# Kernel optimization log

Measured on AMD Instinct MI355X. Metric: run time of the kernel, lower is better.

The kernel has to match this reference:

```python
import jax, jax.numpy as jnp
import numpy as np
from jax import lax

TOP_K = 2

def _unfold(x_img, k):
    # F.unfold(kernel=k, stride=k): [B,C,H,W] -> [B, C*k*k, L], column index c*k*k + kh*k + kw
    B, C, H, W = x_img.shape
    Hp, Wp = H // k, W // k
    u = x_img.reshape(B, C, Hp, k, Wp, k).transpose(0, 1, 3, 5, 2, 4)
    return u.reshape(B, C * k * k, Hp * Wp)

def _fold(p, k, H, W):
    # F.fold inverse of non-overlapping unfold: [B, C*k*k, L] -> [B,C,H,W]
    B = p.shape[0]
    C = p.shape[1] // (k * k)
    Hp, Wp = H // k, W // k
    u = p.reshape(B, C, k, k, Hp, Wp).transpose(0, 1, 4, 2, 5, 3)
    return u.reshape(B, C, H, W)

def setup_inputs() -> dict:
    key = jax.random.key(0)
    ks = jax.random.split(key, 6)
    B, H, W, C, F, E, P = 8, 64, 64, 384, 1536, 8, 4
    N = H * W
    x = jax.random.normal(ks[0], (B, N, C), dtype=jnp.float32)
    gate_w = jax.random.normal(ks[1], (E, C, P, P), dtype=jnp.float32) * 0.01
    w1 = jax.random.normal(ks[2], (E, C, F), dtype=jnp.float32) * (1.0 / np.sqrt(C))
    b1 = jax.random.normal(ks[3], (E, F), dtype=jnp.float32) * 0.01
    w2 = jax.random.normal(ks[4], (E, F, C), dtype=jnp.float32) * (1.0 / np.sqrt(F))
    b2 = jax.random.normal(ks[5], (E, C), dtype=jnp.float32) * 0.01
    return {"x": x, "gate_w": gate_w, "w1": w1, "b1": b1, "w2": w2, "b2": b2, "H": H, "W": W}

def reference(x, gate_w, w1, b1, w2, b2, H, W):
    B, N, C = x.shape
    E, _, P, _ = gate_w.shape
    k2 = P * P
    Hp, Wp = H // P, W // P
    L = Hp * Wp
    x_img = jnp.transpose(x, (0, 2, 1)).reshape(B, C, H, W)
    # router: strided conv -> logits per patch
    logits_map = lax.conv_general_dilated(
        x_img, gate_w, window_strides=(P, P), padding='VALID',
        dimension_numbers=('NCHW', 'OIHW', 'NCHW'))  # [B,E,Hp,Wp]
    router_logits = jnp.transpose(logits_map, (0, 2, 3, 1)).reshape(B, L, E)
    probs = jax.nn.softmax(router_logits, axis=-1)
    ew, ei = lax.top_k(probs, TOP_K)  # [B,L,topk]
    ew = ew / (jnp.sum(ew, axis=-1, keepdims=True) + 1e-9)
    # expand to token level (faithful to original's reshape/flatten ordering)
    ei_tok = jnp.broadcast_to(ei[:, :, None, :], (B, L, k2, TOP_K)).reshape(-1, TOP_K)
    ew_tok = jnp.broadcast_to(ew[:, :, None, :], (B, L, k2, TOP_K)).reshape(-1, TOP_K)
    # unfold + the original's (scrambled) reshape(B, C, L, k2)
    U = _unfold(x_img, P)  # [B, C*k2, L]
    x_patches = jnp.transpose(U.reshape(B, C, L, k2), (0, 2, 3, 1))  # [B,L,k2,C]
    flat_x = x_patches.reshape(-1, C)  # [T,C], T = B*L*k2
    # combine weights: zero for experts not in top-k == masked dispatch math
    cw = jnp.zeros((flat_x.shape[0], E), dtype=flat_x.dtype)
    for kk in range(TOP_K):
        cw = cw + jax.nn.one_hot(ei_tok[:, kk], E, dtype=flat_x.dtype) * ew_tok[:, kk:kk + 1]
    out = jnp.zeros_like(flat_x)
    for e in range(E):
        h = jax.nn.gelu(flat_x @ w1[e] + b1[e], approximate=False)
        y = h @ w2[e] + b2[e]
        out = out + cw[:, e:e + 1] * y
    # fold back (mirrors original's reshape/permute exactly)
    o = jnp.transpose(out.reshape(B, L, k2, C), (0, 3, 1, 2)).reshape(B, C * k2, L)
    out_img = _fold(o, P, H, W)  # [B,C,H,W]
    # original: output.transpose(1,2).reshape(B,N,C) on NCHW tensor
    output = jnp.transpose(out_img, (0, 2, 1, 3)).reshape(B, N, C)
    return output
```

## Files before the change

### kernel.cpp

```cpp
#include <hip/hip_runtime.h>
#include <hip/hip_bf16.h>

#define BB   8
#define HH   64
#define WWID 64
#define CC   384
#define FF   1536
#define EE   8
#define LL   256
#define MTOTMAX 66560
#define NTMAX   520

typedef unsigned short ushort_t;
typedef __attribute__((ext_vector_type(4))) unsigned short u16x4;
typedef __attribute__((ext_vector_type(8))) short          s16x8;
typedef __attribute__((ext_vector_type(4))) float          f32x4;

__device__ __forceinline__ float bf2f(ushort_t u) {
  union { unsigned int i; float f; } v; v.i = ((unsigned int)u) << 16; return v.f;
}
__device__ __forceinline__ ushort_t f2bf(float f) {
  union { float f; unsigned int i; } v; v.f = f;
  unsigned int u = v.i;
  u += 0x7fffu + ((u >> 16) & 1u);
  return (ushort_t)(u >> 16);
}
__device__ __forceinline__ float gelu_f(float x) {
  float u  = 0.70710678118654752f * x;
  float au = fabsf(u);
  float t  = 1.0f / (1.0f + 0.3275911f * au);
  float poly = t * (0.254829592f + t * (-0.284496736f + t * (1.421413741f +
               t * (-1.453152027f + t * 1.061405429f))));
  float ea = 1.0f - poly * __expf(-au * au);
  float erfv = (x < 0.f) ? -ea : ea;
  return 0.5f * x * (1.0f + erfv);
}

#define GLDS(g, l) __builtin_amdgcn_global_load_lds( \
    (const __attribute__((address_space(1))) void*)(g), \
    (__attribute__((address_space(3))) void*)(l), 16, 0, 0)

__global__ __launch_bounds__(256) void k_transpose(const float* __restrict__ src,
                                                   ushort_t* __restrict__ dst,
                                                   int R, int Cd) {
  __shared__ ushort_t tile[32][33];
  int e  = blockIdx.z;
  int c0 = blockIdx.x * 32, r0 = blockIdx.y * 32;
  int tx = threadIdx.x & 31, ty = threadIdx.x >> 5;
  const float* s = src + (size_t)e * R * Cd;
  ushort_t*    d = dst + (size_t)e * R * Cd;
  #pragma unroll
  for (int i = 0; i < 32; i += 8)
    tile[ty + i][tx] = f2bf(s[(size_t)(r0 + ty + i) * Cd + c0 + tx]);
  __syncthreads();
  #pragma unroll
  for (int i = 0; i < 32; i += 8)
    d[(size_t)(c0 + ty + i) * R + r0 + tx] = tile[tx][ty + i];
}

__global__ __launch_bounds__(256) void k_router(const float* __restrict__ x,
                                                const float* __restrict__ gw,
                                                int* __restrict__ re, float* __restrict__ rw,
                                                int* __restrict__ cnt) {
  int bid = blockIdx.x;
  int b = bid >> 8, l2 = bid & 255;
  int hp = l2 >> 4, wp = l2 & 15;
  int t = threadIdx.x;
  int e = t >> 5, lane = t & 31;
  const float* xb = x + (size_t)b * (HH * WWID) * CC;
  const float* ge = gw + (size_t)e * CC * 16;
  float acc = 0.f;
  for (int c = lane; c < CC; c += 32) {
    const float* gp = ge + c * 16;
    #pragma unroll
    for (int kh = 0; kh < 4; ++kh) {
      const float* xr = xb + (size_t)((hp * 4 + kh) * 64 + wp * 4) * CC + c;
      #pragma unroll
      for (int kw = 0; kw < 4; ++kw)
        acc += xr[(size_t)kw * CC] * gp[kh * 4 + kw];
    }
  }
  #pragma unroll
  for (int d = 16; d; d >>= 1) acc += __shfl_down(acc, d, 32);
  __shared__ float logits[EE];
  if (lane == 0) logits[e] = acc;
  __syncthreads();
  if (t == 0) {
    float m = logits[0];
    #pragma unroll
    for (int i = 1; i < EE; ++i) m = fmaxf(m, logits[i]);
    float p[EE]; float s = 0.f;
    #pragma unroll
    for (int i = 0; i < EE; ++i) { p[i] = __expf(logits[i] - m); s += p[i]; }
    #pragma unroll
    for (int i = 0; i < EE; ++i) p[i] /= s;
    int e0 = 0;
    #pragma unroll
    for (int i = 1; i < EE; ++i) if (p[i] > p[e0]) e0 = i;
    int e1 = (e0 == 0) ? 1 : 0;
    #pragma unroll
    for (int i = 0; i < EE; ++i) if (i != e0 && p[i] > p[e1]) e1 = i;
    float s2 = p[e0] + p[e1] + 1e-9f;
    re[bid * 2 + 0] = e0;  re[bid * 2 + 1] = e1;
    rw[bid * 2 + 0] = p[e0] / s2;  rw[bid * 2 + 1] = p[e1] / s2;
    atomicAdd(&cnt[e0], 16);
    atomicAdd(&cnt[e1], 16);
  }
}

__global__ void k_pad(const int* __restrict__ cnt, int* __restrict__ cntp,
                      int* __restrict__ basep, int* __restrict__ tile2e,
                      int* __restrict__ gids, float* __restrict__ gwts) {
  __shared__ int s_cnt[EE], s_cntp[EE], s_base[EE + 1];
  int t = threadIdx.x;
  if (t == 0) {
    int b = 0;
    for (int e = 0; e < EE; ++e) {
      int c  = cnt[e];
      int cp = (c + 127) & ~127;
      s_cnt[e] = c; s_cntp[e] = cp; s_base[e] = b;
      b += cp;
    }
    s_base[EE] = b;
  }
  __syncthreads();
  if (t < EE) { cntp[t] = s_cntp[t]; basep[t] = s_base[t]; }
  if (t == EE) basep[EE] = s_base[EE];
  int ntot = s_base[EE] >> 7;
  for (int g = t; g < ntot; g += 256) {
    int e = 0;
    #pragma unroll
    for (int i = 1; i < EE; ++i) if (g * 128 >= s_base[i]) e = i;
    tile2e[g] = e;
  }
  for (int e = 0; e < EE; ++e)
    for (int i = s_cnt[e] + t; i < s_cntp[e]; i += 256) {
      gids[s_base[e] + i] = -1;
      gwts[s_base[e] + i] = 0.f;
    }
}

__global__ void k_assign(const int* __restrict__ re, const float* __restrict__ rw,
                         const int* __restrict__ basep, int* __restrict__ cnt2,
                         int* __restrict__ gids, float* __restrict__ gwts) {
  int i = blockIdx.x * blockDim.x + threadIdx.x;
  if (i >= BB * LL * 2) return;
  int pat = i >> 1, slot = i & 1;
  int b = pat >> 8, l2 = pat & 255;
  int e = re[i];
  float w = rw[i];
  int t2 = l2 >> 4, hp = l2 & 15;
  int kh = t2 >> 2, kw = t2 & 3;
  int h = hp * 4 + kh;
  int row = basep[e] + atomicAdd(&cnt2[e], 16);
  #pragma unroll
  for (int j = 0; j < 16; ++j) {
    int wpix = j * 4 + kw;
    int pix = (b << 12) + (h << 6) + wpix;
    gids[row + j] = (slot << 15) | pix;
    gwts[row + j] = w;
  }
}

__global__ __launch_bounds__(256) void k_gather(const float* __restrict__ x,
                                                const int* __restrict__ gids,
                                                const int* __restrict__ basep,
                                                ushort_t* __restrict__ Xc, int t0) {
  int g = t0 + blockIdx.x;
  if (g * 128 >= basep[EE]) return;
  __shared__ int s_id[128];
  int t = threadIdx.x;
  if (t < 128) s_id[t] = gids[g * 128 + t];
  __syncthreads();
  ushort_t* dst = Xc + (size_t)blockIdx.x * 128 * CC;
  for (int i = t; i < 128 * 96; i += 256) {
    int row = i / 96, ch = (i % 96) * 4;
    int id = s_id[row];
    f32x4 v = (f32x4){0.f, 0.f, 0.f, 0.f};
    if (id >= 0) v = *reinterpret_cast<const f32x4*>(x + (size_t)(id & 32767) * CC + ch);
    u16x4 o = {f2bf(v.x), f2bf(v.y), f2bf(v.z), f2bf(v.w)};
    *reinterpret_cast<u16x4*>(dst + (size_t)row * CC + ch) = o;
  }
}

__global__ __launch_bounds__(256, 4) void k_gemm1(const ushort_t* __restrict__ Xc,
                                                  const ushort_t* __restrict__ w1t,
                                                  const float* __restrict__ b1,
                                                  const int* __restrict__ basep,
                                                  const int* __restrict__ tile2e,
                                                  ushort_t* __restrict__ Hc, int t0) {
  int g = t0 + blockIdx.y;
  if (g * 128 >= basep[EE]) return;
  int e = tile2e[g], nb = blockIdx.x;
  __shared__ ushort_t As[4096];
  __shared__ ushort_t Bs[4096];
  __shared__ ushort_t tbuf[4][64 * 34];
  int t = threadIdx.x, w = t >> 6, lane = t & 63;
  int l15 = lane & 15, q = lane >> 4;
  const ushort_t* a_src = Xc + (size_t)blockIdx.y * 128 * CC;
  const ushort_t* b_src = w1t + ((size_t)e * FF + nb * 128) * CC;
  int mh = (w & 1) * 4, nh = (w >> 1) * 4;
  f32x4 acc[4][4];
  #pragma unroll
  for (int i = 0; i < 4; ++i)
    #pragma unroll
    for (int j = 0; j < 4; ++j) acc[i][j] = (f32x4){0.f, 0.f, 0.f, 0.f};

  for (int k0 = 0; k0 < CC; k0 += 32) {
    __syncthreads();
    #pragma unroll
    for (int c = 0; c < 2; ++c) {
      int ch = w * 2 + c;
      GLDS(a_src + (size_t)(ch * 16 + l15) * CC + k0 + q * 8, As + ch * 512);
      GLDS(b_src + (size_t)(ch * 16 + l15) * CC + k0 + q * 8, Bs + ch * 512);
    }
    __syncthreads();
    s16x8 af[4], bf[4];
    #pragma unroll
    for (int i = 0; i < 4; ++i)
      af[i] = *reinterpret_cast<const s16x8*>(As + (mh + i) * 512 + lane * 8);
    #pragma unroll
    for (int j = 0; j < 4; ++j)
      bf[j] = *reinterpret_cast<const s16x8*>(Bs + (nh + j) * 512 + lane * 8);
    #pragma unroll
    for (int i = 0; i < 4; ++i)
      #pragma unroll
      for (int j = 0; j < 4; ++j)
        acc[i][j] = __builtin_amdgcn_mfma_f32_16x16x32_bf16(af[i], bf[j], acc[i][j], 0, 0, 0);
  }

  ushort_t* hbase = Hc + (size_t)blockIdx.y * 128 * FF + nb * 128;
  int m0 = (w & 1) * 64, n0 = (w >> 1) * 64;
  ushort_t* tb = &tbuf[w][0];
  int rowi = lane >> 2, fch = (lane & 3) * 8;
  #pragma unroll
  for (int half = 0; half < 2; ++half) {
    #pragma unroll
    for (int jj = 0; jj < 2; ++jj) {
      int j = half * 2 + jj;
      float bj = b1[e * FF + nb * 128 + n0 + j * 16 + l15];
      #pragma unroll
      for (int i = 0; i < 4; ++i)
        #pragma unroll
        for (int r = 0; r < 4; ++r)
          tb[(i * 16 + q * 4 + r) * 34 + jj * 16 + l15] = f2bf(gelu_f(acc[i][j][r] + bj));
    }
    #pragma unroll
    for (int rr = 0; rr < 4; ++rr) {
      int m_loc = rr * 16 + rowi;
      s16x8 v = *reinterpret_cast<const s16x8*>(tb + m_loc * 34 + fch);
      *reinterpret_cast<s16x8*>(hbase + (size_t)(m0 + m_loc) * FF + n0 + half * 32 + fch) = v;
    }
  }
}

__global__ __launch_bounds__(256, 4) void k_gemm2(const ushort_t* __restrict__ Hc,
                                                  const ushort_t* __restrict__ w2t,
                                                  const float* __restrict__ b2,
                                                  const int* __restrict__ basep,
                                                  const int* __restrict__ tile2e,
                                                  const int* __restrict__ gids,
                                                  const float* __restrict__ gwts,
                                                  ushort_t* __restrict__ y, int t0) {
  int g = t0 + blockIdx.y;
  if (g * 128 >= basep[EE]) return;
  int e = tile2e[g], nb = blockIdx.x;
  __shared__ ushort_t As[4096];
  __shared__ ushort_t Bs[4096];
  __shared__ ushort_t tbuf[4][64 * 34];
  __shared__ int   s_id[128];
  __shared__ float s_w[128];
  int t = threadIdx.x, w = t >> 6, lane = t & 63;
  int l15 = lane & 15, q = lane >> 4;
  if (t < 128) {
    s_id[t] = gids[g * 128 + t];
    s_w[t]  = gwts[g * 128 + t];
  }
  const ushort_t* a_src = Hc + (size_t)blockIdx.y * 128 * FF;
  const ushort_t* b_src = w2t + ((size_t)e * CC + nb * 128) * FF;
  int mh = (w & 1) * 4, nh = (w >> 1) * 4;
  f32x4 acc[4][4];
  #pragma unroll
  for (int i = 0; i < 4; ++i)
    #pragma unroll
    for (int j = 0; j < 4; ++j) acc[i][j] = (f32x4){0.f, 0.f, 0.f, 0.f};

  for (int k0 = 0; k0 < FF; k0 += 32) {
    __syncthreads();
    #pragma unroll
    for (int c = 0; c < 2; ++c) {
      int ch = w * 2 + c;
      GLDS(a_src + (size_t)(ch * 16 + l15) * FF + k0 + q * 8, As + ch * 512);
      GLDS(b_src + (size_t)(ch * 16 + l15) * FF + k0 + q * 8, Bs + ch * 512);
    }
    __syncthreads();
    s16x8 af[4], bf[4];
    #pragma unroll
    for (int i = 0; i < 4; ++i)
      af[i] = *reinterpret_cast<const s16x8*>(As + (mh + i) * 512 + lane * 8);
    #pragma unroll
    for (int j = 0; j < 4; ++j)
      bf[j] = *reinterpret_cast<const s16x8*>(Bs + (nh + j) * 512 + lane * 8);
    #pragma unroll
    for (int i = 0; i < 4; ++i)
      #pragma unroll
      for (int j = 0; j < 4; ++j)
        acc[i][j] = __builtin_amdgcn_mfma_f32_16x16x32_bf16(af[i], bf[j], acc[i][j], 0, 0, 0);
  }

  int m0 = (w & 1) * 64, n0 = (w >> 1) * 64;
  ushort_t* tb = &tbuf[w][0];
  int rowi = lane >> 2, fch = (lane & 3) * 8;
  float wrow[4][4];
  #pragma unroll
  for (int i = 0; i < 4; ++i)
    #pragma unroll
    for (int r = 0; r < 4; ++r) wrow[i][r] = s_w[m0 + i * 16 + q * 4 + r];
  #pragma unroll
  for (int half = 0; half < 2; ++half) {
    #pragma unroll
    for (int jj = 0; jj < 2; ++jj) {
      int j = half * 2 + jj;
      float bj = b2[e * CC + nb * 128 + n0 + j * 16 + l15];
      #pragma unroll
      for (int i = 0; i < 4; ++i)
        #pragma unroll
        for (int r = 0; r < 4; ++r)
          tb[(i * 16 + q * 4 + r) * 34 + jj * 16 + l15] = f2bf((acc[i][j][r] + bj) * wrow[i][r]);
    }
    #pragma unroll
    for (int rr = 0; rr < 4; ++rr) {
      int m_loc = rr * 16 + rowi;
      int id = s_id[m0 + m_loc];
      if (id >= 0) {
        s16x8 v = *reinterpret_cast<const s16x8*>(tb + m_loc * 34 + fch);
        *reinterpret_cast<s16x8*>(y + (size_t)id * CC + nb * 128 + n0 + half * 32 + fch) = v;
      }
    }
  }
}

__global__ __launch_bounds__(256) void k_final(const ushort_t* __restrict__ y,
                                               float* __restrict__ out) {
  int bid = blockIdx.x;
  __shared__ float tile[64][193];
  int t = threadIdx.x;
  float* dst = out + (size_t)bid * CC * WWID;
  #pragma unroll
  for (int half = 0; half < 2; ++half) {
    int c0 = half * 192;
    for (int i = t; i < 64 * 48; i += 256) {
      int w = i / 48, c4 = (i % 48) * 4;
      int pix = (bid << 6) + w;
      u16x4 a = *reinterpret_cast<const u16x4*>(y + (size_t)pix * CC + c0 + c4);
      u16x4 b = *reinterpret_cast<const u16x4*>(y + (size_t)(32768 + pix) * CC + c0 + c4);
      #pragma unroll
      for (int k = 0; k < 4; ++k)
        tile[w][c4 + k] = bf2f(a[k]) + bf2f(b[k]);
    }
    __syncthreads();
    for (int i = t; i < 64 * 192; i += 256) {
      int cl = i / 64, w = i % 64;
      dst[(size_t)(c0 + cl) * WWID + w] = tile[w][cl];
    }
    __syncthreads();
  }
}

extern "C" void kernel_launch(void* const* d_in, const int* in_sizes, int n_in,
                              void* d_out, int out_size, void* d_ws, size_t ws_size,
                              hipStream_t stream) {
  const float* x  = (const float*)d_in[0];
  const float* gw = (const float*)d_in[1];
  const float* w1 = (const float*)d_in[2];
  const float* b1 = (const float*)d_in[3];
  const float* w2 = (const float*)d_in[4];
  const float* b2 = (const float*)d_in[5];

  const size_t fixed = (size_t)EE * FF * CC * 2 * 2
                     + (size_t)65536 * CC * 2
                     + (size_t)MTOTMAX * 4 * 2
                     + (size_t)BB * LL * 2 * 4 * 2
                     + (size_t)NTMAX * 4
                     + 1024;
  const int cands[7] = {66560, 32768, 16384, 8192, 4096, 2048, 1024};
  int MC = 1024;
  for (int i = 0; i < 7; ++i)
    if (fixed + (size_t)cands[i] * 3840 <= ws_size) { MC = cands[i]; break; }
  const int npass = (MTOTMAX + MC - 1) / MC;
  const int ntile = MC / 128;

  char* ws = (char*)d_ws;
  size_t off = 0;
  ushort_t* Xc   = (ushort_t*)(ws + off); off += (size_t)MC * CC * 2;
  ushort_t* Hc   = (ushort_t*)(ws + off); off += (size_t)MC * FF * 2;
  ushort_t* w1t  = (ushort_t*)(ws + off); off += (size_t)EE * FF * CC * 2;
  ushort_t* w2t  = (ushort_t*)(ws + off); off += (size_t)EE * FF * CC * 2;
  ushort_t* y    = (ushort_t*)(ws + off); off += (size_t)65536 * CC * 2;
  int*   gids  = (int*)(ws + off);   off += (size_t)MTOTMAX * 4;
  float* gwts  = (float*)(ws + off); off += (size_t)MTOTMAX * 4;
  int*   re    = (int*)(ws + off);   off += (size_t)BB * LL * 2 * 4;
  float* rw    = (float*)(ws + off); off += (size_t)BB * LL * 2 * 4;
  int*   tile2e= (int*)(ws + off);   off += (size_t)NTMAX * 4;
  int*   cnt   = (int*)(ws + off);   off += 64;
  int*   cnt2  = (int*)(ws + off);   off += 64;
  int*   cntp  = (int*)(ws + off);   off += 64;
  int*   basep = (int*)(ws + off);   off += 64;

  hipMemsetAsync(cnt, 0, 128, stream);

  k_transpose<<<dim3(FF / 32, CC / 32, EE), 256, 0, stream>>>(w1, w1t, CC, FF);
  k_transpose<<<dim3(CC / 32, FF / 32, EE), 256, 0, stream>>>(w2, w2t, FF, CC);
  k_router<<<BB * LL, 256, 0, stream>>>(x, gw, re, rw, cnt);
  k_pad<<<1, 256, 0, stream>>>(cnt, cntp, basep, tile2e, gids, gwts);
  k_assign<<<16, 256, 0, stream>>>(re, rw, basep, cnt2, gids, gwts);

  for (int p = 0; p < npass; ++p) {
    int t0 = p * ntile;
    k_gather<<<ntile, 256, 0, stream>>>(x, gids, basep, Xc, t0);
    k_gemm1<<<dim3(FF / 128, ntile), 256, 0, stream>>>(Xc, w1t, b1, basep, tile2e, Hc, t0);
    k_gemm2<<<dim3(CC / 128, ntile), 256, 0, stream>>>(Hc, w2t, b2, basep, tile2e, gids, gwts, y, t0);
  }
  k_final<<<BB * HH, 256, 0, stream>>>(y, (float*)d_out);
}
```

Baseline: 705.3 us.

## Swap GEMM operand roles for direct epilogue stores and vectorize router

```diff
diff --git a/kernel.cpp b/kernel.cpp
--- a/kernel.cpp
+++ b/kernel.cpp
@@ -58,8 +58,16 @@
     d[(size_t)(c0 + ty + i) * R + r0 + tx] = tile[tx][ty + i];
 }
 
+__global__ void k_tgw(const float* __restrict__ gw, float* __restrict__ gwt) {
+  int e = blockIdx.x, t = threadIdx.x;
+  for (int i = t; i < CC * 16; i += 256) {
+    int c = i >> 4, p = i & 15;
+    gwt[((size_t)e * 16 + p) * CC + c] = gw[(size_t)e * CC * 16 + i];
+  }
+}
+
 __global__ __launch_bounds__(256) void k_router(const float* __restrict__ x,
-                                                const float* __restrict__ gw,
+                                                const float* __restrict__ gwt,
                                                 int* __restrict__ re, float* __restrict__ rw,
                                                 int* __restrict__ cnt) {
   int bid = blockIdx.x;
@@ -68,16 +76,18 @@
   int t = threadIdx.x;
   int e = t >> 5, lane = t & 31;
   const float* xb = x + (size_t)b * (HH * WWID) * CC;
-  const float* ge = gw + (size_t)e * CC * 16;
+  const float* ge = gwt + (size_t)e * 16 * CC;
   float acc = 0.f;
-  for (int c = lane; c < CC; c += 32) {
-    const float* gp = ge + c * 16;
-    #pragma unroll
-    for (int kh = 0; kh < 4; ++kh) {
-      const float* xr = xb + (size_t)((hp * 4 + kh) * 64 + wp * 4) * CC + c;
-      #pragma unroll
-      for (int kw = 0; kw < 4; ++kw)
-        acc += xr[(size_t)kw * CC] * gp[kh * 4 + kw];
+  #pragma unroll
+  for (int p = 0; p < 16; ++p) {
+    int pix = (hp * 4 + (p >> 2)) * 64 + wp * 4 + (p & 3);
+    const float* xr = xb + (size_t)pix * CC;
+    const float* gr = ge + (size_t)p * CC;
+    #pragma unroll
+    for (int it = 0; it < 3; ++it) {
+      f32x4 xv = *reinterpret_cast<const f32x4*>(xr + it * 128 + lane * 4);
+      f32x4 gv = *reinterpret_cast<const f32x4*>(gr + it * 128 + lane * 4);
+      acc += xv.x * gv.x + xv.y * gv.y + xv.z * gv.z + xv.w * gv.w;
     }
   }
   #pragma unroll
@@ -194,12 +204,11 @@
   int e = tile2e[g], nb = blockIdx.x;
   __shared__ ushort_t As[4096];
   __shared__ ushort_t Bs[4096];
-  __shared__ ushort_t tbuf[4][64 * 34];
   int t = threadIdx.x, w = t >> 6, lane = t & 63;
   int l15 = lane & 15, q = lane >> 4;
-  const ushort_t* a_src = Xc + (size_t)blockIdx.y * 128 * CC;
-  const ushort_t* b_src = w1t + ((size_t)e * FF + nb * 128) * CC;
-  int mh = (w & 1) * 4, nh = (w >> 1) * 4;
+  const ushort_t* a_src = w1t + ((size_t)e * FF + nb * 128) * CC;
+  const ushort_t* b_src = Xc + (size_t)blockIdx.y * 128 * CC;
+  int fh = (w & 1) * 4, mh = (w >> 1) * 4;
   f32x4 acc[4][4];
   #pragma unroll
   for (int i = 0; i < 4; ++i)
@@ -218,10 +227,10 @@
     s16x8 af[4], bf[4];
     #pragma unroll
     for (int i = 0; i < 4; ++i)
-      af[i] = *reinterpret_cast<const s16x8*>(As + (mh + i) * 512 + lane * 8);
+      af[i] = *reinterpret_cast<const s16x8*>(As + (fh + i) * 512 + lane * 8);
     #pragma unroll
     for (int j = 0; j < 4; ++j)
-      bf[j] = *reinterpret_cast<const s16x8*>(Bs + (nh + j) * 512 + lane * 8);
+      bf[j] = *reinterpret_cast<const s16x8*>(Bs + (mh + j) * 512 + lane * 8);
     #pragma unroll
     for (int i = 0; i < 4; ++i)
       #pragma unroll
@@ -229,27 +238,23 @@
         acc[i][j] = __builtin_amdgcn_mfma_f32_16x16x32_bf16(af[i], bf[j], acc[i][j], 0, 0, 0);
   }
 
-  ushort_t* hbase = Hc + (size_t)blockIdx.y * 128 * FF + nb * 128;
-  int m0 = (w & 1) * 64, n0 = (w >> 1) * 64;
-  ushort_t* tb = &tbuf[w][0];
-  int rowi = lane >> 2, fch = (lane & 3) * 8;
-  #pragma unroll
-  for (int half = 0; half < 2; ++half) {
-    #pragma unroll
-    for (int jj = 0; jj < 2; ++jj) {
-      int j = half * 2 + jj;
-      float bj = b1[e * FF + nb * 128 + n0 + j * 16 + l15];
+  ushort_t* hbase = Hc + (size_t)blockIdx.y * 128 * FF;
+  int fb = nb * 128 + fh * 16 + q * 4;
+  f32x4 bias[4];
+  #pragma unroll
+  for (int i = 0; i < 4; ++i)
+    bias[i] = *reinterpret_cast<const f32x4*>(b1 + (size_t)e * FF + fb + i * 16);
+  #pragma unroll
+  for (int j = 0; j < 4; ++j) {
+    int m = mh * 16 + j * 16 + l15;
+    ushort_t* hp = hbase + (size_t)m * FF + fb;
+    #pragma unroll
+    for (int i = 0; i < 4; ++i) {
+      u16x4 v;
       #pragma unroll
-      for (int i = 0; i < 4; ++i)
-        #pragma unroll
-        for (int r = 0; r < 4; ++r)
-          tb[(i * 16 + q * 4 + r) * 34 + jj * 16 + l15] = f2bf(gelu_f(acc[i][j][r] + bj));
-    }
-    #pragma unroll
-    for (int rr = 0; rr < 4; ++rr) {
-      int m_loc = rr * 16 + rowi;
-      s16x8 v = *reinterpret_cast<const s16x8*>(tb + m_loc * 34 + fch);
-      *reinterpret_cast<s16x8*>(hbase + (size_t)(m0 + m_loc) * FF + n0 + half * 32 + fch) = v;
+      for (int r = 0; r < 4; ++r)
+        v[r] = f2bf(gelu_f(acc[i][j][r] + bias[i][r]));
+      *reinterpret_cast<u16x4*>(hp + i * 16) = v;
     }
   }
 }
@@ -267,7 +272,6 @@
   int e = tile2e[g], nb = blockIdx.x;
   __shared__ ushort_t As[4096];
   __shared__ ushort_t Bs[4096];
-  __shared__ ushort_t tbuf[4][64 * 34];
   __shared__ int   s_id[128];
   __shared__ float s_w[128];
   int t = threadIdx.x, w = t >> 6, lane = t & 63;
@@ -276,9 +280,9 @@
     s_id[t] = gids[g * 128 + t];
     s_w[t]  = gwts[g * 128 + t];
   }
-  const ushort_t* a_src = Hc + (size_t)blockIdx.y * 128 * FF;
-  const ushort_t* b_src = w2t + ((size_t)e * CC + nb * 128) * FF;
-  int mh = (w & 1) * 4, nh = (w >> 1) * 4;
+  const ushort_t* a_src = w2t + ((size_t)e * CC + nb * 128) * FF;
+  const ushort_t* b_src = Hc + (size_t)blockIdx.y * 128 * FF;
+  int chh = (w & 1) * 4, mh = (w >> 1) * 4;
   f32x4 acc[4][4];
   #pragma unroll
   for (int i = 0; i < 4; ++i)
@@ -297,10 +301,10 @@
     s16x8 af[4], bf[4];
     #pragma unroll
     for (int i = 0; i < 4; ++i)
-      af[i] = *reinterpret_cast<const s16x8*>(As + (mh + i) * 512 + lane * 8);
+      af[i] = *reinterpret_cast<const s16x8*>(As + (chh + i) * 512 + lane * 8);
     #pragma unroll
     for (int j = 0; j < 4; ++j)
-      bf[j] = *reinterpret_cast<const s16x8*>(Bs + (nh + j) * 512 + lane * 8);
+      bf[j] = *reinterpret_cast<const s16x8*>(Bs + (mh + j) * 512 + lane * 8);
     #pragma unroll
     for (int i = 0; i < 4; ++i)
       #pragma unroll
@@ -308,33 +312,25 @@
         acc[i][j] = __builtin_amdgcn_mfma_f32_16x16x32_bf16(af[i], bf[j], acc[i][j], 0, 0, 0);
   }
 
-  int m0 = (w & 1) * 64, n0 = (w >> 1) * 64;
-  ushort_t* tb = &tbuf[w][0];
-  int rowi = lane >> 2, fch = (lane & 3) * 8;
-  float wrow[4][4];
+  int cb = nb * 128 + chh * 16 + q * 4;
+  f32x4 bias[4];
   #pragma unroll
   for (int i = 0; i < 4; ++i)
-    #pragma unroll
-    for (int r = 0; r < 4; ++r) wrow[i][r] = s_w[m0 + i * 16 + q * 4 + r];
-  #pragma unroll
-  for (int half = 0; half < 2; ++half) {
-    #pragma unroll
-    for (int jj = 0; jj < 2; ++jj) {
-      int j = half * 2 + jj;
-      float bj = b2[e * CC + nb * 128 + n0 + j * 16 + l15];
+    bias[i] = *reinterpret_cast<const f32x4*>(b2 + (size_t)e * CC + cb + i * 16);
+  #pragma unroll
+  for (int j = 0; j < 4; ++j) {
+    int ml = mh * 16 + j * 16 + l15;
+    int id = s_id[ml];
+    if (id >= 0) {
+      float wt = s_w[ml];
+      ushort_t* yp = y + (size_t)id * CC + cb;
       #pragma unroll
-      for (int i = 0; i < 4; ++i)
+      for (int i = 0; i < 4; ++i) {
+        u16x4 v;
         #pragma unroll
         for (int r = 0; r < 4; ++r)
-          tb[(i * 16 + q * 4 + r) * 34 + jj * 16 + l15] = f2bf((acc[i][j][r] + bj) * wrow[i][r]);
-    }
-    #pragma unroll
-    for (int rr = 0; rr < 4; ++rr) {
-      int m_loc = rr * 16 + rowi;
-      int id = s_id[m0 + m_loc];
-      if (id >= 0) {
-        s16x8 v = *reinterpret_cast<const s16x8*>(tb + m_loc * 34 + fch);
-        *reinterpret_cast<s16x8*>(y + (size_t)id * CC + nb * 128 + n0 + half * 32 + fch) = v;
+          v[r] = f2bf((acc[i][j][r] + bias[i][r]) * wt);
+        *reinterpret_cast<u16x4*>(yp + i * 16) = v;
       }
     }
   }
@@ -379,13 +375,14 @@
 
   const size_t fixed = (size_t)EE * FF * CC * 2 * 2
                      + (size_t)65536 * CC * 2
+                     + (size_t)EE * 16 * CC * 4
                      + (size_t)MTOTMAX * 4 * 2
                      + (size_t)BB * LL * 2 * 4 * 2
                      + (size_t)NTMAX * 4
                      + 1024;
-  const int cands[7] = {66560, 32768, 16384, 8192, 4096, 2048, 1024};
+  const int cands[10] = {66560, 57344, 49152, 40960, 32768, 16384, 8192, 4096, 2048, 1024};
   int MC = 1024;
-  for (int i = 0; i < 7; ++i)
+  for (int i = 0; i < 10; ++i)
     if (fixed + (size_t)cands[i] * 3840 <= ws_size) { MC = cands[i]; break; }
   const int npass = (MTOTMAX + MC - 1) / MC;
   const int ntile = MC / 128;
@@ -397,6 +394,7 @@
   ushort_t* w1t  = (ushort_t*)(ws + off); off += (size_t)EE * FF * CC * 2;
   ushort_t* w2t  = (ushort_t*)(ws + off); off += (size_t)EE * FF * CC * 2;
   ushort_t* y    = (ushort_t*)(ws + off); off += (size_t)65536 * CC * 2;
+  float* gwt   = (float*)(ws + off); off += (size_t)EE * 16 * CC * 4;
   int*   gids  = (int*)(ws + off);   off += (size_t)MTOTMAX * 4;
   float* gwts  = (float*)(ws + off); off += (size_t)MTOTMAX * 4;
   int*   re    = (int*)(ws + off);   off += (size_t)BB * LL * 2 * 4;
@@ -411,7 +409,8 @@
 
   k_transpose<<<dim3(FF / 32, CC / 32, EE), 256, 0, stream>>>(w1, w1t, CC, FF);
   k_transpose<<<dim3(CC / 32, FF / 32, EE), 256, 0, stream>>>(w2, w2t, FF, CC);
-  k_router<<<BB * LL, 256, 0, stream>>>(x, gw, re, rw, cnt);
+  k_tgw<<<EE, 256, 0, stream>>>(gw, gwt);
+  k_router<<<BB * LL, 256, 0, stream>>>(x, gwt, re, rw, cnt);
   k_pad<<<1, 256, 0, stream>>>(cnt, cntp, basep, tile2e, gids, gwts);
   k_assign<<<16, 256, 0, stream>>>(re, rw, basep, cnt2, gids, gwts);
 
```

Result: slower. 797.6 us (+13.1%).
